# Optimization experiments

Hardware: AMD Instinct MI355X
Metric: run time of the kernel (lower is better)

The kernel has to match this reference:

```python
import jax, jax.numpy as jnp
import numpy as np


def setup_inputs() -> dict:
    key = jax.random.key(0)
    ks = jax.random.split(key, 8)
    N, E = 10000, 160000
    IN, OUT, TC = 512, 512, 256
    x = jax.random.normal(ks[0], (N, IN), dtype=jnp.float32)
    t_emb = jax.random.normal(ks[1], (TC,), dtype=jnp.float32)
    edge_index = jax.random.randint(ks[2], (2, E), 0, N, dtype=jnp.int64)
    # GCNConv weight (glorot-ish scale) and bias
    W = jax.random.normal(ks[3], (IN, OUT), dtype=jnp.float32) / np.sqrt(IN)
    b = jnp.zeros((OUT,), dtype=jnp.float32)
    # time_proj Linear(TC, OUT)
    Wt = jax.random.normal(ks[4], (TC, OUT), dtype=jnp.float32) / np.sqrt(TC)
    bt = jnp.zeros((OUT,), dtype=jnp.float32)
    return {"x": x, "t_emb": t_emb, "edge_index": edge_index,
            "W": W, "b": b, "Wt": Wt, "bt": bt}


def _gcn_conv(x, edge_index, W, b):
    # PyG GCNConv: add self-loops, symmetric normalization, xW, scatter-add, +bias
    N = x.shape[0]
    loops = jnp.arange(N, dtype=edge_index.dtype)
    src = jnp.concatenate([edge_index[0], loops])  # [E+N]
    dst = jnp.concatenate([edge_index[1], loops])
    deg = jax.ops.segment_sum(jnp.ones_like(dst, dtype=x.dtype), dst,
                              num_segments=N)  # in-degree incl. self-loop
    dinv = jnp.where(deg > 0, jax.lax.rsqrt(deg), 0.0)
    norm = dinv[src] * dinv[dst]  # [E+N]
    xw = x @ W  # [N, OUT] - transform before gather (fewer FLOPs on edges)
    msgs = norm[:, None] * xw[src]  # [E+N, OUT]
    out = jax.ops.segment_sum(msgs, dst, num_segments=N)
    return out + b


def reference(x, t_emb, edge_index, W, b, Wt, bt):
    h = _gcn_conv(x, edge_index, W, b)          # [N, OUT]
    time_emb = t_emb @ Wt + bt                   # [OUT] (1-D t_emb branch)
    return h + time_emb
```

## Files before the change

### kernel.cpp

```cpp
#include <hip/hip_runtime.h>

#define OUTC 512
#define INC 512
#define NTILE 4
#define TCOL 128
#define LDA 72
#define TPB 256

typedef __bf16 bf16x8 __attribute__((ext_vector_type(8)));
typedef float f32x4 __attribute__((ext_vector_type(4)));

static __device__ __forceinline__ unsigned short f2bf(float f) {
    unsigned u = __float_as_uint(f);
    unsigned r = u + 0x7fffu + ((u >> 16) & 1u);
    return (unsigned short)(r >> 16);
}
static __device__ __forceinline__ float bflo(unsigned r) { return __uint_as_float(r << 16); }
static __device__ __forceinline__ float bfhi(unsigned r) { return __uint_as_float(r & 0xffff0000u); }
static __device__ __forceinline__ void acc8s(float* a, uint4 v, float n) {
    a[0] += n * bflo(v.x); a[1] += n * bfhi(v.x);
    a[2] += n * bflo(v.y); a[3] += n * bfhi(v.y);
    a[4] += n * bflo(v.z); a[5] += n * bfhi(v.z);
    a[6] += n * bflo(v.w); a[7] += n * bfhi(v.w);
}

__global__ void k_zero(int* __restrict__ p, int n) {
    int i = blockIdx.x * 256 + threadIdx.x;
    if (i < n) p[i] = 0;
}

__global__ __launch_bounds__(256) void k_prep(const float* __restrict__ x,
                                              const float* __restrict__ W,
                                              const float* __restrict__ t_emb,
                                              const float* __restrict__ Wt,
                                              const float* __restrict__ bt,
                                              const float* __restrict__ b,
                                              const int* __restrict__ dst,
                                              int* __restrict__ counts,
                                              unsigned short* __restrict__ xb,
                                              unsigned short* __restrict__ wtb,
                                              float* __restrict__ temb,
                                              int E, int CB, int XBB,
                                              int M, int Mpad, int TC) {
    __shared__ float smem[32 * 33];
    int bid = blockIdx.x;
    if (bid < CB) {
        int e = bid * 256 + threadIdx.x;
        if (e < E) atomicAdd(&counts[dst[e]], 1);
    } else if (bid < CB + XBB) {
        int idx = (bid - CB) * 256 + threadIdx.x;
        int row = idx >> 6;
        int kg = (idx & 63) * 8;
        ushort4 h0 = make_ushort4(0, 0, 0, 0), h1 = make_ushort4(0, 0, 0, 0);
        if (row < M) {
            float4 v0 = *(const float4*)(x + (size_t)row * INC + kg);
            float4 v1 = *(const float4*)(x + (size_t)row * INC + kg + 4);
            h0 = make_ushort4(f2bf(v0.x), f2bf(v0.y), f2bf(v0.z), f2bf(v0.w));
            h1 = make_ushort4(f2bf(v1.x), f2bf(v1.y), f2bf(v1.z), f2bf(v1.w));
        }
        *(ushort4*)(xb + (size_t)row * INC + kg) = h0;
        *(ushort4*)(xb + (size_t)row * INC + kg + 4) = h1;
    } else if (bid < CB + XBB + 256) {
        int b2 = bid - (CB + XBB);
        int bk = (b2 & 15) * 32, bn = (b2 >> 4) * 32;
        int tx = threadIdx.x & 31, ty = threadIdx.x >> 5;
        for (int r = ty; r < 32; r += 8)
            smem[r * 33 + tx] = W[(size_t)(bk + r) * OUTC + bn + tx];
        __syncthreads();
        for (int r = ty; r < 32; r += 8)
            wtb[(size_t)(bn + r) * INC + bk + tx] = f2bf(smem[tx * 33 + r]);
    } else {
        int j = bid - (CB + XBB + 256);
        int t = threadIdx.x;
        float p = 0.0f;
        for (int k = t; k < TC; k += 256) p += t_emb[k] * Wt[(size_t)k * OUTC + j];
        smem[t] = p;
        __syncthreads();
        for (int s = 128; s > 0; s >>= 1) {
            if (t < s) smem[t] += smem[t + s];
            __syncthreads();
        }
        if (t == 0) temb[j] = smem[0] + bt[j] + b[j];
    }
}

__global__ __launch_bounds__(256) void k_ag(const unsigned short* __restrict__ xb,
                                            const unsigned short* __restrict__ wtb,
                                            unsigned short* __restrict__ xwb,
                                            const int* __restrict__ counts,
                                            int* __restrict__ row_start,
                                            int* __restrict__ cursor,
                                            float* __restrict__ dinv,
                                            int* __restrict__ allocCtr,
                                            int N, int Mpad) {
    __shared__ unsigned short la[128 * LDA];
    __shared__ unsigned short lb[64 * LDA];

    const int bid = blockIdx.x;
    const int tid = threadIdx.x;
    const int GB = (Mpad / 128) * 8;

    if (bid >= GB) {
        const int lane = tid & 63;
        const int gwave = ((bid - GB) * TPB + tid) >> 6;
        for (int c0 = gwave * 64; c0 < N; c0 += 160 * 64) {
            int d = c0 + lane;
            int deg = (d < N) ? counts[d] : 0;
            int incl = deg;
#pragma unroll
            for (int off = 1; off < 64; off <<= 1) {
                int v = __shfl_up(incl, off, 64);
                if (lane >= off) incl += v;
            }
            int wtot = __shfl(incl, 63, 64);
            int base = 0;
            if (lane == 63) base = atomicAdd(allocCtr, wtot);
            base = __shfl(base, 63, 64);
            if (d < N) {
                int rs = base + incl - deg;
                row_start[d] = rs;
                cursor[d] = rs;
                dinv[d] = rsqrtf((float)deg + 1.0f);
            }
        }
        return;
    }

    const int n0 = (bid & 7) * 64;
    const int m0 = (bid >> 3) * 128;
    const int lane = tid & 63;
    const int wave = tid >> 6;
    const int wm = wave * 32;
    const int l15 = lane & 15;
    const int k8 = (lane >> 4) * 8;

    f32x4 acc[2][4];
#pragma unroll
    for (int t = 0; t < 2; ++t)
#pragma unroll
        for (int u = 0; u < 4; ++u)
            acc[t][u] = (f32x4){0.f, 0.f, 0.f, 0.f};

    for (int k0 = 0; k0 < INC; k0 += 64) {
#pragma unroll
        for (int i = 0; i < 4; ++i) {
            int f = i * 256 + tid;
            int row = f >> 3, c = f & 7;
            uint4 v = *(const uint4*)(xb + (size_t)(m0 + row) * INC + k0 + c * 8);
            *(uint4*)(&la[row * LDA + c * 8]) = v;
        }
#pragma unroll
        for (int i = 0; i < 2; ++i) {
            int f = i * 256 + tid;
            int row = f >> 3, c = f & 7;
            uint4 v = *(const uint4*)(wtb + (size_t)(n0 + row) * INC + k0 + c * 8);
            *(uint4*)(&lb[row * LDA + c * 8]) = v;
        }
        __syncthreads();

#pragma unroll
        for (int kc = 0; kc < 64; kc += 32) {
            bf16x8 af0 = *(const bf16x8*)(&la[(wm + l15) * LDA + kc + k8]);
            bf16x8 af1 = *(const bf16x8*)(&la[(wm + 16 + l15) * LDA + kc + k8]);
#pragma unroll
            for (int u = 0; u < 4; ++u) {
                bf16x8 bfr = *(const bf16x8*)(&lb[(u * 16 + l15) * LDA + kc + k8]);
                acc[0][u] = __builtin_amdgcn_mfma_f32_16x16x32_bf16(af0, bfr, acc[0][u], 0, 0, 0);
                acc[1][u] = __builtin_amdgcn_mfma_f32_16x16x32_bf16(af1, bfr, acc[1][u], 0, 0, 0);
            }
        }
        __syncthreads();
    }

    const int rbase = (lane >> 4) * 4;
#pragma unroll
    for (int t = 0; t < 2; ++t)
#pragma unroll
        for (int u = 0; u < 4; ++u) {
            int gcol = n0 + u * 16 + l15;
            unsigned short* p = xwb + (size_t)(gcol >> 7) * Mpad * TCOL + (gcol & 127);
#pragma unroll
            for (int r = 0; r < 4; ++r) {
                int grow = m0 + wm + t * 16 + rbase + r;
                p[(size_t)grow * TCOL] = f2bf(acc[t][u][r]);
            }
        }
}

__global__ void k_scatter(const int* __restrict__ src, const int* __restrict__ dst,
                          const float* __restrict__ dinv,
                          int* __restrict__ cursor, int2* __restrict__ epk, int E) {
    int e = blockIdx.x * blockDim.x + threadIdx.x;
    if (e < E) {
        int s = src[e];
        int d = dst[e];
        int pos = atomicAdd(&cursor[d], 1);
        epk[pos] = make_int2(s, __float_as_int(dinv[s]));
    }
}

__global__ __launch_bounds__(256) void k_gather(const int2* __restrict__ epk,
                                                const int* __restrict__ row_start,
                                                const int* __restrict__ counts,
                                                const unsigned short* __restrict__ xwb,
                                                const float* __restrict__ dinv,
                                                const float* __restrict__ temb,
                                                float* __restrict__ out, int N, int Mpad) {
    const int bid = blockIdx.x;
    const int tile = (bid & 7) >> 1;
    const int node = (bid >> 3) * 8 + (bid & 1) * 4 + (threadIdx.x >> 6);
    if (node >= N) return;
    const int lane = threadIdx.x & 63;
    const int slot = lane >> 4;
    const int c8 = (lane & 15) * 8;
    const unsigned short* basep = xwb + (size_t)tile * Mpad * TCOL + c8;

    float a[8] = {0.f, 0.f, 0.f, 0.f, 0.f, 0.f, 0.f, 0.f};
    const int s0 = row_start[node];
    const int s1 = s0 + counts[node];
    int i = s0;
    for (; i + 8 <= s1; i += 8) {
        int2 eA = epk[i + slot];
        int2 eB = epk[i + 4 + slot];
        float nA = __int_as_float(eA.y);
        float nB = __int_as_float(eB.y);
        uint4 vA = *(const uint4*)(basep + (size_t)eA.x * TCOL);
        uint4 vB = *(const uint4*)(basep + (size_t)eB.x * TCOL);
        acc8s(a, vA, nA);
        acc8s(a, vB, nB);
    }
    for (; i < s1; i += 4) {
        int idx = i + slot;
        int sA = node;
        float nA = 0.f;
        if (idx < s1) {
            int2 e = epk[idx];
            sA = e.x;
            nA = __int_as_float(e.y);
        }
        uint4 v = *(const uint4*)(basep + (size_t)sA * TCOL);
        acc8s(a, v, nA);
    }
#pragma unroll
    for (int k = 0; k < 8; ++k) {
        a[k] += __shfl_xor(a[k], 16, 64);
        a[k] += __shfl_xor(a[k], 32, 64);
    }
    const float di = dinv[node];
    {
        uint4 v = *(const uint4*)(basep + (size_t)node * TCOL);
        acc8s(a, v, di);
    }
    if (slot < 2) {
        const int gc = tile * TCOL + c8 + slot * 4;
        float4 tv = *(const float4*)(temb + gc);
        float4 o;
        o.x = di * a[slot * 4 + 0] + tv.x;
        o.y = di * a[slot * 4 + 1] + tv.y;
        o.z = di * a[slot * 4 + 2] + tv.z;
        o.w = di * a[slot * 4 + 3] + tv.w;
        *(float4*)(out + (size_t)node * OUTC + gc) = o;
    }
}

extern "C" void kernel_launch(void* const* d_in, const int* in_sizes, int n_in,
                              void* d_out, int out_size, void* d_ws, size_t ws_size,
                              hipStream_t stream) {
    const float* x     = (const float*)d_in[0];
    const float* t_emb = (const float*)d_in[1];
    const int*   ei    = (const int*)d_in[2];
    const float* W     = (const float*)d_in[3];
    const float* b     = (const float*)d_in[4];
    const float* Wt    = (const float*)d_in[5];
    const float* bt    = (const float*)d_in[6];
    float* out = (float*)d_out;

    const int N  = in_sizes[0] / INC;
    const int E  = in_sizes[2] / 2;
    const int TC = in_sizes[1];
    const int Mpad = (N + 127) & ~127;

    char* ws = (char*)d_ws;
    size_t off = 0;
    unsigned short* xb  = (unsigned short*)(ws + off); off += (size_t)Mpad * INC * 2;
    unsigned short* xwb = (unsigned short*)(ws + off); off += (size_t)Mpad * OUTC * 2;
    unsigned short* wtb = (unsigned short*)(ws + off); off += (size_t)INC * OUTC * 2;
    float* dinv = (float*)(ws + off);      off += ((size_t)N * 4 + 255) & ~(size_t)255;
    int* counts = (int*)(ws + off);        off += ((size_t)(N + 1) * 4 + 255) & ~(size_t)255;
    int* allocCtr = counts + N;
    int* row_start = (int*)(ws + off);     off += ((size_t)N * 4 + 255) & ~(size_t)255;
    int* cursor = (int*)(ws + off);        off += ((size_t)N * 4 + 255) & ~(size_t)255;
    int2* epk = (int2*)(ws + off);         off += ((size_t)(E + 64) * 8 + 255) & ~(size_t)255;
    float* temb = (float*)(ws + off);      off += OUTC * 4;

    const int* srcIdx = ei;
    const int* dstIdx = ei + E;

    const int CB  = (E + 255) / 256;
    const int XBB = Mpad * (INC / 8) / 256;
    const int GB  = (Mpad / 128) * 8;

    k_zero<<<(N + 1 + 255) / 256, TPB, 0, stream>>>(counts, N + 1);
    k_prep<<<CB + XBB + 256 + OUTC, TPB, 0, stream>>>(x, W, t_emb, Wt, bt, b, dstIdx,
                                                      counts, xb, wtb, temb,
                                                      E, CB, XBB, N, Mpad, TC);
    k_ag<<<GB + 40, TPB, 0, stream>>>(xb, wtb, xwb, counts, row_start, cursor,
                                      dinv, allocCtr, N, Mpad);
    k_scatter<<<(E + 255) / 256, TPB, 0, stream>>>(srcIdx, dstIdx, dinv, cursor, epk, E);

    const int gather_blocks = ((N + 7) / 8) * 8;
    k_gather<<<gather_blocks, TPB, 0, stream>>>(epk, row_start, counts, xwb, dinv,
                                                temb, out, N, Mpad);
}
```

Before: 148.0 us.

## Fuse x bf16 conversion into GEMM tile load and co-schedule edge scatter with GEMM

Removes the separate x-to-bf16 pass and its workspace buffer. The GEMM now reads fp32 x directly and converts to bf16 while filling shared memory. The CSR allocation scan becomes its own small kernel, and the edge scatter blocks are merged into the GEMM launch so scatter and matrix multiply run concurrently. This saves a full read and write of x in bf16 and one launch, at the cost of doubled global load width in the GEMM tile loop and an extra launch for the scan.

```diff
diff --git a/kernel.cpp b/kernel.cpp
--- a/kernel.cpp
+++ b/kernel.cpp
@@ -29,39 +29,23 @@
     if (i < n) p[i] = 0;
 }
 
-__global__ __launch_bounds__(256) void k_prep(const float* __restrict__ x,
-                                              const float* __restrict__ W,
+__global__ __launch_bounds__(256) void k_prep(const float* __restrict__ W,
                                               const float* __restrict__ t_emb,
                                               const float* __restrict__ Wt,
                                               const float* __restrict__ bt,
                                               const float* __restrict__ b,
                                               const int* __restrict__ dst,
                                               int* __restrict__ counts,
-                                              unsigned short* __restrict__ xb,
                                               unsigned short* __restrict__ wtb,
                                               float* __restrict__ temb,
-                                              int E, int CB, int XBB,
-                                              int M, int Mpad, int TC) {
+                                              int E, int CB, int TC) {
     __shared__ float smem[32 * 33];
     int bid = blockIdx.x;
     if (bid < CB) {
         int e = bid * 256 + threadIdx.x;
         if (e < E) atomicAdd(&counts[dst[e]], 1);
-    } else if (bid < CB + XBB) {
-        int idx = (bid - CB) * 256 + threadIdx.x;
-        int row = idx >> 6;
-        int kg = (idx & 63) * 8;
-        ushort4 h0 = make_ushort4(0, 0, 0, 0), h1 = make_ushort4(0, 0, 0, 0);
-        if (row < M) {
-            float4 v0 = *(const float4*)(x + (size_t)row * INC + kg);
-            float4 v1 = *(const float4*)(x + (size_t)row * INC + kg + 4);
-            h0 = make_ushort4(f2bf(v0.x), f2bf(v0.y), f2bf(v0.z), f2bf(v0.w));
-            h1 = make_ushort4(f2bf(v1.x), f2bf(v1.y), f2bf(v1.z), f2bf(v1.w));
-        }
-        *(ushort4*)(xb + (size_t)row * INC + kg) = h0;
-        *(ushort4*)(xb + (size_t)row * INC + kg + 4) = h1;
-    } else if (bid < CB + XBB + 256) {
-        int b2 = bid - (CB + XBB);
+    } else if (bid < CB + 256) {
+        int b2 = bid - CB;
         int bk = (b2 & 15) * 32, bn = (b2 >> 4) * 32;
         int tx = threadIdx.x & 31, ty = threadIdx.x >> 5;
         for (int r = ty; r < 32; r += 8)
@@ -70,7 +54,7 @@
         for (int r = ty; r < 32; r += 8)
             wtb[(size_t)(bn + r) * INC + bk + tx] = f2bf(smem[tx * 33 + r]);
     } else {
-        int j = bid - (CB + XBB + 256);
+        int j = bid - (CB + 256);
         int t = threadIdx.x;
         float p = 0.0f;
         for (int k = t; k < TC; k += 256) p += t_emb[k] * Wt[(size_t)k * OUTC + j];
@@ -84,50 +68,64 @@
     }
 }
 
-__global__ __launch_bounds__(256) void k_ag(const unsigned short* __restrict__ xb,
+__global__ __launch_bounds__(256) void k_alloc(const int* __restrict__ counts,
+                                               int* __restrict__ row_start,
+                                               int* __restrict__ cursor,
+                                               float* __restrict__ dinv,
+                                               int* __restrict__ allocCtr, int N) {
+    const int lane = threadIdx.x & 63;
+    const int gwave = (blockIdx.x * TPB + threadIdx.x) >> 6;
+    for (int c0 = gwave * 64; c0 < N; c0 += 160 * 64) {
+        int d = c0 + lane;
+        int deg = (d < N) ? counts[d] : 0;
+        int incl = deg;
+#pragma unroll
+        for (int off = 1; off < 64; off <<= 1) {
+            int v = __shfl_up(incl, off, 64);
+            if (lane >= off) incl += v;
+        }
+        int wtot = __shfl(incl, 63, 64);
+        int base = 0;
+        if (lane == 63) base = atomicAdd(allocCtr, wtot);
+        base = __shfl(base, 63, 64);
+        if (d < N) {
+            int rs = base + incl - deg;
+            row_start[d] = rs;
+            cursor[d] = rs;
+            dinv[d] = rsqrtf((float)deg + 1.0f);
+        }
+    }
+}
+
+__global__ __launch_bounds__(256) void k_sg(const float* __restrict__ x,
                                             const unsigned short* __restrict__ wtb,
                                             unsigned short* __restrict__ xwb,
-                                            const int* __restrict__ counts,
-                                            int* __restrict__ row_start,
+                                            const int* __restrict__ src,
+                                            const int* __restrict__ dst,
+                                            const float* __restrict__ dinv,
                                             int* __restrict__ cursor,
-                                            float* __restrict__ dinv,
-                                            int* __restrict__ allocCtr,
-                                            int N, int Mpad) {
+                                            int2* __restrict__ epk,
+                                            int N, int E, int Mpad, int SB) {
     __shared__ unsigned short la[128 * LDA];
     __shared__ unsigned short lb[64 * LDA];
 
     const int bid = blockIdx.x;
     const int tid = threadIdx.x;
-    const int GB = (Mpad / 128) * 8;
-
-    if (bid >= GB) {
-        const int lane = tid & 63;
-        const int gwave = ((bid - GB) * TPB + tid) >> 6;
-        for (int c0 = gwave * 64; c0 < N; c0 += 160 * 64) {
-            int d = c0 + lane;
-            int deg = (d < N) ? counts[d] : 0;
-            int incl = deg;
-#pragma unroll
-            for (int off = 1; off < 64; off <<= 1) {
-                int v = __shfl_up(incl, off, 64);
-                if (lane >= off) incl += v;
-            }
-            int wtot = __shfl(incl, 63, 64);
-            int base = 0;
-            if (lane == 63) base = atomicAdd(allocCtr, wtot);
-            base = __shfl(base, 63, 64);
-            if (d < N) {
-                int rs = base + incl - deg;
-                row_start[d] = rs;
-                cursor[d] = rs;
-                dinv[d] = rsqrtf((float)deg + 1.0f);
-            }
+
+    if (bid < SB) {
+        int e = bid * 256 + tid;
+        if (e < E) {
+            int s = src[e];
+            int d = dst[e];
+            int pos = atomicAdd(&cursor[d], 1);
+            epk[pos] = make_int2(s, __float_as_int(dinv[s]));
         }
         return;
     }
 
-    const int n0 = (bid & 7) * 64;
-    const int m0 = (bid >> 3) * 128;
+    const int gb = bid - SB;
+    const int n0 = (gb & 7) * 64;
+    const int m0 = (gb >> 3) * 128;
     const int lane = tid & 63;
     const int wave = tid >> 6;
     const int wm = wave * 32;
@@ -143,11 +141,14 @@
 
     for (int k0 = 0; k0 < INC; k0 += 64) {
 #pragma unroll
-        for (int i = 0; i < 4; ++i) {
+        for (int i = 0; i < 8; ++i) {
             int f = i * 256 + tid;
-            int row = f >> 3, c = f & 7;
-            uint4 v = *(const uint4*)(xb + (size_t)(m0 + row) * INC + k0 + c * 8);
-            *(uint4*)(&la[row * LDA + c * 8]) = v;
+            int row = f >> 4, c4 = f & 15;
+            int gm = m0 + row;
+            float4 v = make_float4(0.f, 0.f, 0.f, 0.f);
+            if (gm < N) v = *(const float4*)(x + (size_t)gm * INC + k0 + c4 * 4);
+            ushort4 h = make_ushort4(f2bf(v.x), f2bf(v.y), f2bf(v.z), f2bf(v.w));
+            *(ushort4*)(&la[row * LDA + c4 * 4]) = h;
         }
 #pragma unroll
         for (int i = 0; i < 2; ++i) {
@@ -185,18 +186,6 @@
                 p[(size_t)grow * TCOL] = f2bf(acc[t][u][r]);
             }
         }
-}
-
-__global__ void k_scatter(const int* __restrict__ src, const int* __restrict__ dst,
-                          const float* __restrict__ dinv,
-                          int* __restrict__ cursor, int2* __restrict__ epk, int E) {
-    int e = blockIdx.x * blockDim.x + threadIdx.x;
-    if (e < E) {
-        int s = src[e];
-        int d = dst[e];
-        int pos = atomicAdd(&cursor[d], 1);
-        epk[pos] = make_int2(s, __float_as_int(dinv[s]));
-    }
 }
 
 __global__ __launch_bounds__(256) void k_gather(const int2* __restrict__ epk,
@@ -282,7 +271,6 @@
 
     char* ws = (char*)d_ws;
     size_t off = 0;
-    unsigned short* xb  = (unsigned short*)(ws + off); off += (size_t)Mpad * INC * 2;
     unsigned short* xwb = (unsigned short*)(ws + off); off += (size_t)Mpad * OUTC * 2;
     unsigned short* wtb = (unsigned short*)(ws + off); off += (size_t)INC * OUTC * 2;
     float* dinv = (float*)(ws + off);      off += ((size_t)N * 4 + 255) & ~(size_t)255;
@@ -296,17 +284,16 @@
     const int* srcIdx = ei;
     const int* dstIdx = ei + E;
 
-    const int CB  = (E + 255) / 256;
-    const int XBB = Mpad * (INC / 8) / 256;
-    const int GB  = (Mpad / 128) * 8;
+    const int CB = (E + 255) / 256;
+    const int SB = ((E + 255) / 256 + 7) & ~7;
+    const int GB = (Mpad / 128) * 8;
 
     k_zero<<<(N + 1 + 255) / 256, TPB, 0, stream>>>(counts, N + 1);
-    k_prep<<<CB + XBB + 256 + OUTC, TPB, 0, stream>>>(x, W, t_emb, Wt, bt, b, dstIdx,
-                                                      counts, xb, wtb, temb,
-                                                      E, CB, XBB, N, Mpad, TC);
-    k_ag<<<GB + 40, TPB, 0, stream>>>(xb, wtb, xwb, counts, row_start, cursor,
-                                      dinv, allocCtr, N, Mpad);
-    k_scatter<<<(E + 255) / 256, TPB, 0, stream>>>(srcIdx, dstIdx, dinv, cursor, epk, E);
+    k_prep<<<CB + 256 + OUTC, TPB, 0, stream>>>(W, t_emb, Wt, bt, b, dstIdx,
+                                                counts, wtb, temb, E, CB, TC);
+    k_alloc<<<40, TPB, 0, stream>>>(counts, row_start, cursor, dinv, allocCtr, N);
+    k_sg<<<SB + GB, TPB, 0, stream>>>(x, wtb, xwb, srcIdx, dstIdx, dinv, cursor, epk,
+                                      N, E, Mpad, SB);
 
     const int gather_blocks = ((N + 7) / 8) * 8;
     k_gather<<<gather_blocks, TPB, 0, stream>>>(epk, row_start, counts, xwb, dinv,
```

Result: slower. 165.5 us (+11.8%).
